# Optimization experiments

Hardware: AMD Instinct MI355X
Metric: run time of the kernel (lower is better)

Reference implementation:

```python
import jax, jax.numpy as jnp
import numpy as np

NODE_DIM = 128; EDGE_DIM = 64; TIME_DIM = 32; HIDDEN = 256; N_LAYERS = 2
K = 20; N_NODES = 100000; B = 8192
IN_DIM = 2 * NODE_DIM + EDGE_DIM + TIME_DIM  # 352


def time2vec(t, w0, b0, w, b):
    # t: [...] -> [..., TIME_DIM]; linear term + sinusoidal terms (Time2Vec)
    t = t[..., None]
    return jnp.concatenate([w0 * t + b0, jnp.sin(w * t + b)], axis=-1)


def msg_mlp(x, W1, b1, W2, b2):
    # TemporalMessageFunction: Linear -> ReLU -> Linear
    return jax.nn.relu(x @ W1 + b1) @ W2 + b2


def gru_cell(x, h, w_ih, w_hh, b_ih, b_hh):
    # torch.nn.GRUCell math, gate order (r, z, n)
    gx = x @ w_ih.T + b_ih
    gh = h @ w_hh.T + b_hh
    rx, zx, nx = jnp.split(gx, 3, axis=-1)
    rh, zh, nh = jnp.split(gh, 3, axis=-1)
    r = jax.nn.sigmoid(rx + rh)
    z = jax.nn.sigmoid(zx + zh)
    n = jnp.tanh(nx + r * nh)
    return (1.0 - z) * n + z * h


def setup_inputs():
    key = jax.random.key(0)
    ks = jax.random.split(key, 24)
    def rn(i, shape, scale=1.0):
        return jax.random.normal(ks[i], shape, dtype=jnp.float32) * scale
    return {
        "src_nodes": jax.random.randint(ks[0], (B,), 0, N_NODES),
        "dst_nodes": jax.random.randint(ks[1], (B,), 0, N_NODES),
        "edge_attrs": rn(2, (B, EDGE_DIM)),
        "timestamps": jax.random.uniform(ks[3], (B,), dtype=jnp.float32) * 1000.0,
        "memory": rn(4, (N_NODES, NODE_DIM), 0.1),
        "neighbor_ids": jax.random.randint(ks[5], (N_NODES, K), 0, N_NODES),
        "neighbor_times": jax.random.uniform(ks[6], (N_NODES, K), dtype=jnp.float32) * 1000.0,
        "neighbor_edge_attrs": rn(7, (N_NODES, K, EDGE_DIM), 0.1),
        "t2v_w0": rn(8, (1,)),
        "t2v_b0": rn(9, (1,)),
        "t2v_w": rn(10, (TIME_DIM - 1,)),
        "t2v_b": rn(11, (TIME_DIM - 1,)),
        "enc_W": rn(12, (EDGE_DIM, EDGE_DIM), EDGE_DIM ** -0.5),
        "enc_b": rn(13, (EDGE_DIM,), 0.01),
        "mlp_W1": rn(14, (N_LAYERS, IN_DIM, HIDDEN), IN_DIM ** -0.5),
        "mlp_b1": rn(15, (N_LAYERS, HIDDEN), 0.01),
        "mlp_W2": rn(16, (N_LAYERS, HIDDEN, NODE_DIM), HIDDEN ** -0.5),
        "mlp_b2": rn(17, (N_LAYERS, NODE_DIM), 0.01),
        "gru_w_ih": rn(18, (3 * NODE_DIM, NODE_DIM), NODE_DIM ** -0.5),
        "gru_w_hh": rn(19, (3 * NODE_DIM, NODE_DIM), NODE_DIM ** -0.5),
        "gru_b_ih": rn(20, (3 * NODE_DIM,), 0.01),
        "gru_b_hh": rn(21, (3 * NODE_DIM,), 0.01),
    }


def reference(src_nodes, dst_nodes, edge_attrs, timestamps, memory,
              neighbor_ids, neighbor_times, neighbor_edge_attrs,
              t2v_w0, t2v_b0, t2v_w, t2v_b, enc_W, enc_b,
              mlp_W1, mlp_b1, mlp_W2, mlp_b2,
              gru_w_ih, gru_w_hh, gru_b_ih, gru_b_hh):
    time_emb = time2vec(timestamps, t2v_w0, t2v_b0, t2v_w, t2v_b)  # [B, T]
    edge_enc = edge_attrs @ enc_W + enc_b                           # [B, E]
    src_emb = memory[src_nodes]                                     # [B, D]
    dst_emb = memory[dst_nodes]                                     # [B, D]

    def neighbor_agg(node_ids, layer):
        # gather K temporal neighbors per node, run message MLP, mean-aggregate
        nb_ids = neighbor_ids[node_ids]                 # [B, K]
        nb_emb = memory[nb_ids]                         # [B, K, D]
        node_mem = jnp.broadcast_to(memory[node_ids][:, None, :], nb_emb.shape)
        nb_t = time2vec(neighbor_times[node_ids], t2v_w0, t2v_b0, t2v_w, t2v_b)  # [B, K, T]
        nb_e = neighbor_edge_attrs[node_ids]            # [B, K, E]
        x = jnp.concatenate([nb_emb, node_mem, nb_e, nb_t], axis=-1)  # [B, K, IN_DIM]
        msgs = msg_mlp(x, mlp_W1[layer], mlp_b1[layer], mlp_W2[layer], mlp_b2[layer])
        return msgs.mean(axis=1)                        # [B, D]

    for l in range(N_LAYERS):
        src_nb = neighbor_agg(src_nodes, l)
        dst_nb = neighbor_agg(dst_nodes, l)
        x_src = jnp.concatenate([src_emb, dst_emb, edge_enc, time_emb], axis=-1)
        x_dst = jnp.concatenate([dst_emb, src_emb, edge_enc, time_emb], axis=-1)
        m_src = msg_mlp(x_src, mlp_W1[l], mlp_b1[l], mlp_W2[l], mlp_b2[l]) + src_nb
        m_dst = msg_mlp(x_dst, mlp_W1[l], mlp_b1[l], mlp_W2[l], mlp_b2[l]) + dst_nb
        src_emb = gru_cell(m_src, src_emb, gru_w_ih, gru_w_hh, gru_b_ih, gru_b_hh)
        dst_emb = gru_cell(m_dst, dst_emb, gru_w_ih, gru_w_hh, gru_b_ih, gru_b_hh)

    return jnp.concatenate([src_emb, dst_emb], axis=-1)  # [B, 2*D]
```

## Files before the change

### kernel.cpp

```cpp
#include <hip/hip_runtime.h>
#include <math.h>


typedef __bf16 bf16;
typedef __bf16 bf16x8 __attribute__((ext_vector_type(8)));
typedef float f32x4 __attribute__((ext_vector_type(4)));

#define MFMA16(a, b, c) __builtin_amdgcn_mfma_f32_16x16x32_bf16((a), (b), (c), 0, 0, 0)

__device__ __forceinline__ void split2(float v, bf16& hi, bf16& lo) {
  hi = (bf16)v;
  lo = (bf16)(v - (float)hi);
}

__device__ __forceinline__ bf16x8 cvt8(const float* __restrict__ p) {
  float4 a = *(const float4*)p;
  float4 b = *(const float4*)(p + 4);
  bf16x8 r;
  r[0] = (bf16)a.x; r[1] = (bf16)a.y; r[2] = (bf16)a.z; r[3] = (bf16)a.w;
  r[4] = (bf16)b.x; r[5] = (bf16)b.y; r[6] = (bf16)b.z; r[7] = (bf16)b.w;
  return r;
}

#define NB_EV 8192
#define ROWS_NB (NB_EV * 20)
#define N_NODES 100000
#define IN_DIM 352
#define HID 256
#define ND 128

__global__ void k_prep_weights(const float* __restrict__ W1, const float* __restrict__ W2,
                               const float* __restrict__ wih, const float* __restrict__ whh,
                               bf16* __restrict__ W1blk, bf16* __restrict__ W1red,
                               bf16* __restrict__ W2blk,
                               bf16* __restrict__ wihblk, bf16* __restrict__ whhblk,
                               float* __restrict__ w320) {
  const int NW1 = 2 * 11 * 256 * 32;
  const int NW1R = 2 * 7 * 256 * 32;
  const int NW2 = 2 * 2 * 8 * 128 * 32;
  const int NG = 2 * 4 * 384 * 32;
  int total = NW1 + NW1R + NW2 + NG + NG + 512;
  for (int i = blockIdx.x * blockDim.x + threadIdx.x; i < total; i += gridDim.x * blockDim.x) {
    int j = i;
    if (j < NW1) {
      int l = j / 90112, r = j - l * 90112;
      int k0 = r / 8192, r2 = r & 8191;
      int n = r2 >> 5, ko = r2 & 31, k = k0 * 32 + ko;
      W1blk[j] = (bf16)W1[(l * 352 + k) * 256 + n];
    } else if ((j -= NW1) < NW1R) {
      int l = j / 57344, r = j - l * 57344;
      int kq = r / 8192, r2 = r & 8191;
      int n = r2 >> 5, ko = r2 & 31;
      int k = (kq < 4) ? (kq * 32 + ko) : ((kq < 6) ? (256 + (kq - 4) * 32 + ko) : (320 + ko));
      W1red[j] = (bf16)W1[(l * 352 + k) * 256 + n];
    } else if ((j -= NW1R) < NW2) {
      int l = j >> 16, r = j & 65535;
      int plane = r >> 15, r2 = r & 32767;
      int kg = r2 >> 12, r3 = r2 & 4095;
      int n = r3 >> 5, ko = r3 & 31, k = kg * 32 + ko;
      bf16 hi, lo; split2(W2[(l * 256 + k) * 128 + n], hi, lo);
      W2blk[j] = plane ? lo : hi;
    } else if ((j -= NW2) < NG) {
      int plane = j / 49152, r = j - plane * 49152;
      int kg = r / 12288, r2 = r - kg * 12288;
      int n = r2 >> 5, ko = r2 & 31, k = kg * 32 + ko;
      bf16 hi, lo; split2(wih[n * 128 + k], hi, lo);
      wihblk[j] = plane ? lo : hi;
    } else if ((j -= NG) < NG) {
      int plane = j / 49152, r = j - plane * 49152;
      int kg = r / 12288, r2 = r - kg * 12288;
      int n = r2 >> 5, ko = r2 & 31, k = kg * 32 + ko;
      bf16 hi, lo; split2(whh[n * 128 + k], hi, lo);
      whhblk[j] = plane ? lo : hi;
    } else {
      j -= NG;
      int l = j >> 8, n = j & 255;
      w320[j] = W1[(l * 352 + 320) * 256 + n];
    }
  }
}

__global__ void k_prep_misc(const float* __restrict__ ts, const float* __restrict__ w0,
                            const float* __restrict__ b0, const float* __restrict__ w,
                            const float* __restrict__ bb,
                            const int* __restrict__ srcn, const int* __restrict__ dstn,
                            const float* __restrict__ memory,
                            float* __restrict__ time_emb, float* __restrict__ embA0,
                            float* __restrict__ embB0) {
  const int N1 = NB_EV * 32, N2 = NB_EV * ND;
  int total = N1 + N2;
  float w0v = w0[0], b0v = b0[0];
  for (int i = blockIdx.x * blockDim.x + threadIdx.x; i < total; i += gridDim.x * blockDim.x) {
    int j = i;
    if (j < N1) {
      int b = j >> 5, c = j & 31;
      float t = ts[b];
      time_emb[j] = (c == 0) ? (w0v * t + b0v) : sinf(w[c - 1] * t + bb[c - 1]);
    } else {
      j -= N1;
      int b = j >> 7, c = j & 127;
      embA0[j] = memory[(long)srcn[b] * ND + c];
      embB0[j] = memory[(long)dstn[b] * ND + c];
    }
  }
}

__global__ void k_prep_mem(const float* __restrict__ memory, bf16* __restrict__ memB) {
  long total = (long)N_NODES * ND / 8;
  for (long i = blockIdx.x * blockDim.x + threadIdx.x; i < total; i += (long)gridDim.x * blockDim.x) {
    bf16x8 v = cvt8(memory + i * 8);
    *(bf16x8*)&memB[i * 8] = v;
  }
}

__global__ __launch_bounds__(256) void k_prep_nbr(
    const int* __restrict__ srcn, const int* __restrict__ dstn,
    const int* __restrict__ nbids, const float* __restrict__ nbt,
    const float* __restrict__ nbe,
    const float* __restrict__ w0p, const float* __restrict__ b0p,
    const float* __restrict__ wp, const float* __restrict__ bp,
    bf16* __restrict__ Xlin, int* __restrict__ nbidArr, float* __restrict__ clArr) {
  __shared__ int flat_l[64];
  __shared__ float t_l[64];
  const int tid = threadIdx.x;
  const int side = blockIdx.y;
  const int r0 = blockIdx.x * 64;
  const int* nodes = side ? dstn : srcn;
  if (tid < 64) {
    int rg = r0 + tid;
    int b = rg / 20, k = rg - b * 20;
    int n = nodes[b];
    int flat = n * 20 + k;
    flat_l[tid] = flat;
    nbidArr[side * ROWS_NB + rg] = nbids[flat];
    float t = nbt[flat];
    t_l[tid] = t;
    clArr[side * ROWS_NB + rg] = w0p[0] * t + b0p[0];
  }
  __syncthreads();
  for (int task = tid; task < 64 * 12; task += 256) {
    int r = task / 12, j = task - r * 12;
    bf16x8 v;
    if (j < 8) {
      v = cvt8(nbe + (long)flat_l[r] * 64 + j * 8);
    } else {
      float t = t_l[r];
#pragma unroll
      for (int q = 0; q < 8; ++q) {
        int c = (j - 8) * 8 + q;
        v[q] = (c == 0) ? (bf16)0.f : (bf16)__sinf(wp[c - 1] * t + bp[c - 1]);
      }
    }
    *(bf16x8*)&Xlin[((long)side * ROWS_NB + r0 + r) * 96 + j * 8] = v;
  }
}

__global__ void k_edge(const float* __restrict__ ea, const float* __restrict__ encW,
                       const float* __restrict__ encb, float* __restrict__ out) {
  __shared__ float row[64];
  int b = blockIdx.x, j = threadIdx.x;
  row[j] = ea[b * 64 + j];
  __syncthreads();
  float s = encb[j];
#pragma unroll
  for (int k = 0; k < 64; ++k) s += row[k] * encW[k * 64 + j];
  out[b * 64 + j] = s;
}

__global__ __launch_bounds__(256) void k_hnode(
    const int* __restrict__ srcn, const int* __restrict__ dstn,
    const float* __restrict__ memory, const bf16* __restrict__ W1blk,
    float* __restrict__ Hnode) {
  const int tid = threadIdx.x;
  const int wid = tid >> 6, lane = tid & 63;
  const int colq = lane & 15, cq = lane >> 4;
  const int cq8 = cq * 8;
  const int z = blockIdx.y, layer = z >> 1, side = z & 1;
  const int b0 = blockIdx.x * 64;
  const int* nodes = side ? dstn : srcn;

  long node_r[4];
#pragma unroll
  for (int nr = 0; nr < 4; ++nr) node_r[nr] = nodes[b0 + nr * 16 + colq];

  const bf16* W1l = W1blk + layer * 90112 + 4 * 8192 + (wid * 16 + colq) * 32 + cq8;
  f32x4 acc[4][4];
#pragma unroll
  for (int mc = 0; mc < 4; ++mc)
#pragma unroll
    for (int nr = 0; nr < 4; ++nr) acc[mc][nr] = (f32x4){0.f, 0.f, 0.f, 0.f};
#pragma unroll
  for (int k0 = 0; k0 < 4; ++k0) {
    bf16x8 xb[4];
#pragma unroll
    for (int nr = 0; nr < 4; ++nr)
      xb[nr] = cvt8(memory + node_r[nr] * ND + k0 * 32 + cq8);
    bf16x8 wf[4];
#pragma unroll
    for (int mc = 0; mc < 4; ++mc)
      wf[mc] = *(const bf16x8*)(W1l + k0 * 8192 + mc * 2048);
#pragma unroll
    for (int mc = 0; mc < 4; ++mc)
#pragma unroll
      for (int nr = 0; nr < 4; ++nr)
        acc[mc][nr] = MFMA16(wf[mc], xb[nr], acc[mc][nr]);
  }
#pragma unroll
  for (int mc = 0; mc < 4; ++mc)
#pragma unroll
    for (int nr = 0; nr < 4; ++nr) {
      long row = (long)z * NB_EV + b0 + nr * 16 + colq;
      *(f32x4*)&Hnode[row * 256 + mc * 64 + wid * 16 + cq * 4] = acc[mc][nr];
    }
}

#define HSS2 136
#define F_XS 0
#define F_HHI 35840
#define F_HLO 57600
#define F_CL 79360
#define F_TOT 79680
__global__ __launch_bounds__(256, 2) void k_nbr(
    const bf16* __restrict__ memB, const int* __restrict__ nbidArr,
    const float* __restrict__ clArr, const bf16* __restrict__ Xlin,
    const float* __restrict__ Hnode,
    const bf16* __restrict__ W1red, const bf16* __restrict__ W2blk,
    const float* __restrict__ w320, const float* __restrict__ b1,
    const float* __restrict__ b2, float* __restrict__ nb_out) {
  __shared__ __align__(16) char smem[F_TOT];
  bf16* xs = (bf16*)(smem + F_XS);
  bf16* hhi = (bf16*)(smem + F_HHI);
  bf16* hlo = (bf16*)(smem + F_HLO);
  float* cl = (float*)(smem + F_CL);
  int* nbid_l = (int*)(smem + F_HHI);

  const int tid = threadIdx.x;
  const int wid = tid >> 6, lane = tid & 63;
  const int colq = lane & 15, cq = lane >> 4;
  const int cq8 = cq * 8;
  const int side = blockIdx.y;
  const int r0 = blockIdx.x * 80;

  if (tid < 80) {
    nbid_l[tid] = nbidArr[side * ROWS_NB + r0 + tid];
    cl[tid] = clArr[side * ROWS_NB + r0 + tid];
  }
  __syncthreads();

  float clr[5];
  int ev_r[5];
#pragma unroll
  for (int nr = 0; nr < 5; ++nr) {
    int row = nr * 16 + colq;
    clr[nr] = cl[row];
    ev_r[nr] = blockIdx.x * 4 + row / 20;
  }

  for (int task = tid; task < 80 * 28; task += 256) {
    int r = task / 28, c16 = task - r * 28;
    bf16x8 v;
    int kq, k8;
    if (c16 < 16) {
      v = *(const bf16x8*)&memB[(long)nbid_l[r] * ND + c16 * 8];
      kq = c16 >> 2; k8 = c16 & 3;
    } else {
      int jj = c16 - 16;
      v = *(const bf16x8*)&Xlin[((long)side * ROWS_NB + r0 + r) * 96 + jj * 8];
      kq = (jj < 8) ? (4 + (jj >> 2)) : 6;
      k8 = (jj < 8) ? (jj & 3) : (jj - 8);
    }
    int swz = k8 ^ (r & 3) ^ ((r >> 2) & 3);
    *(bf16x8*)&xs[kq * 2560 + r * 32 + swz * 8] = v;
  }
  __syncthreads();

  const int swzr = cq ^ (colq & 3) ^ ((colq >> 2) & 3);

#pragma unroll
  for (int layer = 0; layer < 2; ++layer) {
    const bf16* W1l = W1red + layer * 57344 + (wid * 16 + colq) * 32 + cq8;
    const float* Hz = Hnode + ((long)(layer * 2 + side) * NB_EV) * 256;

    f32x4 acc[4][5];
#pragma unroll
    for (int mc = 0; mc < 4; ++mc)
#pragma unroll
      for (int nr = 0; nr < 5; ++nr)
        acc[mc][nr] = *(const f32x4*)&Hz[(long)ev_r[nr] * 256 + mc * 64 + wid * 16 + cq * 4];

    bf16x8 w1f[7][4];
#pragma unroll
    for (int kq = 0; kq < 7; ++kq)
#pragma unroll
      for (int mc = 0; mc < 4; ++mc)
        w1f[kq][mc] = *(const bf16x8*)(W1l + kq * 8192 + mc * 2048);
#pragma unroll
    for (int kq = 0; kq < 7; ++kq)
#pragma unroll
      for (int mc = 0; mc < 4; ++mc)
        asm volatile("" : "+v"(w1f[kq][mc]));

#pragma unroll
    for (int kq = 0; kq < 7; ++kq) {
      bf16x8 xb[5];
#pragma unroll
      for (int nr = 0; nr < 5; ++nr)
        xb[nr] = *(const bf16x8*)(xs + kq * 2560 + (nr * 16 + colq) * 32 + swzr * 8);
#pragma unroll
      for (int mc = 0; mc < 4; ++mc)
#pragma unroll
        for (int nr = 0; nr < 5; ++nr)
          acc[mc][nr] = MFMA16(w1f[kq][mc], xb[nr], acc[mc][nr]);
    }

    const float* w320l = w320 + layer * 256;
    const float* b1l = b1 + layer * 256;
#pragma unroll
    for (int mc = 0; mc < 4; ++mc) {
      int c0 = mc * 64 + wid * 16 + cq * 4;
      float4 wv = *(const float4*)&w320l[c0];
      float4 bv = *(const float4*)&b1l[c0];
#pragma unroll
      for (int nr = 0; nr < 5; ++nr) {
        float c = clr[nr];
        acc[mc][nr][0] = fmaxf(acc[mc][nr][0] + c * wv.x + bv.x, 0.f);
        acc[mc][nr][1] = fmaxf(acc[mc][nr][1] + c * wv.y + bv.y, 0.f);
        acc[mc][nr][2] = fmaxf(acc[mc][nr][2] + c * wv.z + bv.z, 0.f);
        acc[mc][nr][3] = fmaxf(acc[mc][nr][3] + c * wv.w + bv.w, 0.f);
      }
    }

    if (layer == 1) __syncthreads();

    const bf16* W2h = W2blk + layer * 65536 + (wid * 32 + colq) * 32 + cq8;
    const bf16* W2l = W2h + 32768;
    f32x4 acc2[2][5];
#pragma unroll
    for (int mc2 = 0; mc2 < 2; ++mc2)
#pragma unroll
      for (int nr = 0; nr < 5; ++nr) acc2[mc2][nr] = (f32x4){0.f, 0.f, 0.f, 0.f};

#pragma unroll
    for (int hh = 0; hh < 2; ++hh) {
#pragma unroll
      for (int mq = 0; mq < 2; ++mq) {
        int mc = hh * 2 + mq;
        int cl0 = mq * 64 + wid * 16 + cq * 4;
#pragma unroll
        for (int nr = 0; nr < 5; ++nr) {
          int r = nr * 16 + colq;
          union { bf16 h[4]; uint2 u; } ph, pl;
#pragma unroll
          for (int i = 0; i < 4; ++i) split2(acc[mc][nr][i], ph.h[i], pl.h[i]);
          *(uint2*)&hhi[r * HSS2 + cl0] = ph.u;
          *(uint2*)&hlo[r * HSS2 + cl0] = pl.u;
        }
      }
      __syncthreads();

      bf16x8 w2hf[4][2], w2lf[4][2];
#pragma unroll
      for (int kq = 0; kq < 4; ++kq)
#pragma unroll
        for (int mc2 = 0; mc2 < 2; ++mc2) {
          w2hf[kq][mc2] = *(const bf16x8*)(W2h + (hh * 4 + kq) * 4096 + mc2 * 512);
          w2lf[kq][mc2] = *(const bf16x8*)(W2l + (hh * 4 + kq) * 4096 + mc2 * 512);
        }
#pragma unroll
      for (int kq = 0; kq < 4; ++kq)
#pragma unroll
        for (int mc2 = 0; mc2 < 2; ++mc2) {
          asm volatile("" : "+v"(w2hf[kq][mc2]));
          asm volatile("" : "+v"(w2lf[kq][mc2]));
        }

#pragma unroll
      for (int kq = 0; kq < 4; ++kq) {
        bf16x8 bh[5], bl[5];
#pragma unroll
        for (int nr = 0; nr < 5; ++nr) {
          int r = nr * 16 + colq;
          bh[nr] = *(const bf16x8*)(hhi + r * HSS2 + kq * 32 + cq8);
          bl[nr] = *(const bf16x8*)(hlo + r * HSS2 + kq * 32 + cq8);
        }
#pragma unroll
        for (int mc2 = 0; mc2 < 2; ++mc2)
#pragma unroll
          for (int nr = 0; nr < 5; ++nr) {
            acc2[mc2][nr] = MFMA16(w2hf[kq][mc2], bh[nr], acc2[mc2][nr]);
            acc2[mc2][nr] = MFMA16(w2lf[kq][mc2], bh[nr], acc2[mc2][nr]);
            acc2[mc2][nr] = MFMA16(w2hf[kq][mc2], bl[nr], acc2[mc2][nr]);
          }
      }
      if (hh == 0) __syncthreads();
    }

    {
      const float* b2l = b2 + layer * 128;
      long zbase = (long)(layer * 2 + side) * NB_EV * ND;
#pragma unroll
      for (int e = 0; e < 4; ++e) {
        int lo = e * 20, hi = lo + 20;
        f32x4 v[2];
#pragma unroll
        for (int mc2 = 0; mc2 < 2; ++mc2) {
          v[mc2] = (f32x4){0.f, 0.f, 0.f, 0.f};
#pragma unroll
          for (int nr = 0; nr < 5; ++nr) {
            int rl = nr * 16 + colq;
            if (rl >= lo && rl < hi) v[mc2] += acc2[mc2][nr];
          }
        }
#pragma unroll
        for (int s = 1; s < 16; s <<= 1) {
#pragma unroll
          for (int mc2 = 0; mc2 < 2; ++mc2) {
            v[mc2][0] += __shfl_xor(v[mc2][0], s);
            v[mc2][1] += __shfl_xor(v[mc2][1], s);
            v[mc2][2] += __shfl_xor(v[mc2][2], s);
            v[mc2][3] += __shfl_xor(v[mc2][3], s);
          }
        }
        if (colq == e) {
          long b = blockIdx.x * 4 + e;
#pragma unroll
          for (int mc2 = 0; mc2 < 2; ++mc2) {
            int c = wid * 32 + mc2 * 16 + cq * 4;
            float4 bv = *(const float4*)&b2l[c];
            float4 o;
            o.x = (v[mc2][0] + 20.f * bv.x) * 0.05f;
            o.y = (v[mc2][1] + 20.f * bv.y) * 0.05f;
            o.z = (v[mc2][2] + 20.f * bv.z) * 0.05f;
            o.w = (v[mc2][3] + 20.f * bv.w) * 0.05f;
            *(float4*)&nb_out[zbase + b * ND + c] = o;
          }
        }
      }
    }
  }
}

#define XSS 360
#define HSS 136
#define E_G 46080
#define E_CL 80896
#define E_TOT 81152
__global__ __launch_bounds__(256, 1) void k_event(
    int layer, const float* __restrict__ embA_in, const float* __restrict__ embB_in,
    float* __restrict__ outA, int ostrideA, float* __restrict__ outB, int ostrideB,
    const float* __restrict__ time_emb, const float* __restrict__ edge_enc,
    const bf16* __restrict__ W1blk, const bf16* __restrict__ W2blk,
    const float* __restrict__ w320, const float* __restrict__ b1,
    const float* __restrict__ b2, const float* __restrict__ nb_out,
    const bf16* __restrict__ wihblk, const bf16* __restrict__ whhblk,
    const float* __restrict__ bih, const float* __restrict__ bhh) {
  __shared__ __align__(16) char smem[E_TOT];
  bf16* xs = (bf16*)(smem);
  bf16* hhi = (bf16*)(smem);
  bf16* hlo = (bf16*)(smem + 17408);
  bf16* mhi = (bf16*)(smem);
  bf16* mlo = (bf16*)(smem + 17408);
  bf16* ghi = (bf16*)(smem + E_G);
  bf16* glo = (bf16*)(smem + E_G + 17408);
  float* cl = (float*)(smem + E_CL);

  const int tid = threadIdx.x;
  const int r0 = blockIdx.x * 64;
  const int side = r0 >> 13;
  const int b0r = r0 & (NB_EV - 1);
  const float* ea = side ? embB_in : embA_in;
  const float* eb = side ? embA_in : embB_in;

  if (tid < 64) cl[tid] = time_emb[(b0r + tid) * 32];

  for (int task = tid; task < 64 * 88; task += 256) {
    int r = task / 88; int c = (task - r * 88) * 4;
    int b = b0r + r;
    float4 v;
    if (c < 128) {
      v = *(const float4*)&ea[(long)b * ND + c];
      bf16 h0, l0, h1, l1, h2, l2, h3, l3;
      split2(v.x, h0, l0); split2(v.y, h1, l1); split2(v.z, h2, l2); split2(v.w, h3, l3);
      ghi[r * HSS + c + 0] = h0; glo[r * HSS + c + 0] = l0;
      ghi[r * HSS + c + 1] = h1; glo[r * HSS + c + 1] = l1;
      ghi[r * HSS + c + 2] = h2; glo[r * HSS + c + 2] = l2;
      ghi[r * HSS + c + 3] = h3; glo[r * HSS + c + 3] = l3;
    } else if (c < 256) {
      v = *(const float4*)&eb[(long)b * ND + (c - 128)];
    } else if (c < 320) {
      v = *(const float4*)&edge_enc[(long)b * 64 + (c - 256)];
    } else {
      float vv[4];
#pragma unroll
      for (int q = 0; q < 4; ++q) {
        int cc = c + q - 320;
        vv[q] = (cc == 0) ? 0.f : time_emb[b * 32 + cc];
      }
      v = make_float4(vv[0], vv[1], vv[2], vv[3]);
    }
    union { bf16 h[4]; uint2 u; } pk;
    pk.h[0] = (bf16)v.x; pk.h[1] = (bf16)v.y; pk.h[2] = (bf16)v.z; pk.h[3] = (bf16)v.w;
    *(uint2*)&xs[r * XSS + c] = pk.u;
  }
  __syncthreads();

  const int wid = tid >> 6, lane = tid & 63;
  const int colq = lane & 15, cq = lane >> 4;
  const int rsub = cq * 4;

  const bf16* W1l = W1blk + layer * 90112 + (wid * 64 + colq) * 32 + cq * 8;
  const bf16* xsl = xs + colq * XSS + cq * 8;
  f32x4 acc[4][4];
#pragma unroll
  for (int m = 0; m < 4; ++m)
#pragma unroll
    for (int n = 0; n < 4; ++n) acc[m][n] = (f32x4){0.f, 0.f, 0.f, 0.f};
#pragma unroll
  for (int k0 = 0; k0 < 11; ++k0) {
    bf16x8 a[4], b[4];
#pragma unroll
    for (int m = 0; m < 4; ++m) a[m] = *(const bf16x8*)(xsl + m * 16 * XSS + k0 * 32);
#pragma unroll
    for (int n = 0; n < 4; ++n) b[n] = *(const bf16x8*)(W1l + k0 * 8192 + n * 512);
#pragma unroll
    for (int m = 0; m < 4; ++m)
#pragma unroll
      for (int n = 0; n < 4; ++n) acc[m][n] = MFMA16(a[m], b[n], acc[m][n]);
  }
  __syncthreads();

  const float* w320l = w320 + layer * 256;
  const float* b1l = b1 + layer * 256;
#pragma unroll
  for (int n = 0; n < 4; ++n) {
    int cg = wid * 64 + n * 16 + colq;
    float wv = w320l[cg], bv = b1l[cg];
#pragma unroll
    for (int m = 0; m < 4; ++m)
#pragma unroll
      for (int i = 0; i < 4; ++i) {
        int r = m * 16 + rsub + i;
        acc[m][n][i] = fmaxf(acc[m][n][i] + cl[r] * wv + bv, 0.f);
      }
  }
  if (wid < 2) {
#pragma unroll
    for (int m = 0; m < 4; ++m)
#pragma unroll
      for (int n = 0; n < 4; ++n)
#pragma unroll
        for (int i = 0; i < 4; ++i) {
          int r = m * 16 + rsub + i;
          int cc = wid * 64 + n * 16 + colq;
          bf16 hi, lo; split2(acc[m][n][i], hi, lo);
          hhi[r * HSS + cc] = hi;
          hlo[r * HSS + cc] = lo;
        }
  }
  __syncthreads();

  const bf16* W2h = W2blk + layer * 65536 + (wid * 32 + colq) * 32 + cq * 8;
  const bf16* W2l = W2h + 32768;
  const bf16* hhil = hhi + colq * HSS + cq * 8;
  const bf16* hlol = hlo + colq * HSS + cq * 8;
  f32x4 acc2[4][2];
#pragma unroll
  for (int m = 0; m < 4; ++m)
#pragma unroll
    for (int n = 0; n < 2; ++n) acc2[m][n] = (f32x4){0.f, 0.f, 0.f, 0.f};
#pragma unroll
  for (int kg = 0; kg < 8; ++kg) {
    if (kg == 4) {
      __syncthreads();
      if (wid >= 2) {
#pragma unroll
        for (int m = 0; m < 4; ++m)
#pragma unroll
          for (int n = 0; n < 4; ++n)
#pragma unroll
            for (int i = 0; i < 4; ++i) {
              int r = m * 16 + rsub + i;
              int cc = (wid & 1) * 64 + n * 16 + colq;
              bf16 hi, lo; split2(acc[m][n][i], hi, lo);
              hhi[r * HSS + cc] = hi;
              hlo[r * HSS + cc] = lo;
            }
      }
      __syncthreads();
    }
    int lk = (kg & 3) * 32;
    bf16x8 ahi[4], alo[4], bhi[2], blo[2];
#pragma unroll
    for (int m = 0; m < 4; ++m) {
      ahi[m] = *(const bf16x8*)(hhil + m * 16 * HSS + lk);
      alo[m] = *(const bf16x8*)(hlol + m * 16 * HSS + lk);
    }
#pragma unroll
    for (int n = 0; n < 2; ++n) {
      bhi[n] = *(const bf16x8*)(W2h + kg * 4096 + n * 512);
      blo[n] = *(const bf16x8*)(W2l + kg * 4096 + n * 512);
    }
#pragma unroll
    for (int m = 0; m < 4; ++m)
#pragma unroll
      for (int n = 0; n < 2; ++n) {
        acc2[m][n] = MFMA16(ahi[m], bhi[n], acc2[m][n]);
        acc2[m][n] = MFMA16(ahi[m], blo[n], acc2[m][n]);
        acc2[m][n] = MFMA16(alo[m], bhi[n], acc2[m][n]);
      }
  }
  __syncthreads();

  const float* b2l = b2 + layer * 128;
  const float* nbl = nb_out + ((long)(layer * 2 + side)) * NB_EV * ND;
#pragma unroll
  for (int n = 0; n < 2; ++n) {
    int cg = wid * 32 + n * 16 + colq;
    float bv = b2l[cg];
#pragma unroll
    for (int m = 0; m < 4; ++m)
#pragma unroll
      for (int i = 0; i < 4; ++i) {
        int r = m * 16 + rsub + i;
        float mval = acc2[m][n][i] + bv + nbl[(long)(b0r + r) * ND + cg];
        bf16 hi, lo; split2(mval, hi, lo);
        mhi[r * HSS + cg] = hi;
        mlo[r * HSS + cg] = lo;
      }
  }
  __syncthreads();

  float* outP = side ? outB : outA;
  const int ostride = side ? ostrideB : ostrideA;
  const int rowA = wid * 16 + colq;
  const int rbase = wid * 16 + rsub;
  const bf16* mhil = mhi + rowA * HSS + cq * 8;
  const bf16* mlol = mlo + rowA * HSS + cq * 8;
  const bf16* ghil = ghi + rowA * HSS + cq * 8;
  const bf16* glol = glo + rowA * HSS + cq * 8;
  const bf16* wihl = wihblk + colq * 32 + cq * 8;
  const bf16* whhl = whhblk + colq * 32 + cq * 8;

  for (int jt = 0; jt < 8; ++jt) {
    f32x4 gx[3], gh[3];
#pragma unroll
    for (int g = 0; g < 3; ++g) {
      gx[g] = (f32x4){0.f, 0.f, 0.f, 0.f};
      gh[g] = (f32x4){0.f, 0.f, 0.f, 0.f};
    }
#pragma unroll
    for (int kc = 0; kc < 4; ++kc) {
      bf16x8 amh = *(const bf16x8*)(mhil + kc * 32);
      bf16x8 aml = *(const bf16x8*)(mlol + kc * 32);
      bf16x8 ahh = *(const bf16x8*)(ghil + kc * 32);
      bf16x8 ahl = *(const bf16x8*)(glol + kc * 32);
#pragma unroll
      for (int g = 0; g < 3; ++g) {
        int nb = (g * 128 + jt * 16) * 32;
        bf16x8 bh = *(const bf16x8*)(wihl + kc * 12288 + nb);
        bf16x8 bl = *(const bf16x8*)(wihl + 49152 + kc * 12288 + nb);
        gx[g] = MFMA16(amh, bh, gx[g]);
        gx[g] = MFMA16(aml, bh, gx[g]);
        gx[g] = MFMA16(amh, bl, gx[g]);
        bf16x8 ch = *(const bf16x8*)(whhl + kc * 12288 + nb);
        bf16x8 cl2 = *(const bf16x8*)(whhl + 49152 + kc * 12288 + nb);
        gh[g] = MFMA16(ahh, ch, gh[g]);
        gh[g] = MFMA16(ahl, ch, gh[g]);
        gh[g] = MFMA16(ahh, cl2, gh[g]);
      }
    }
    int j = jt * 16 + colq;
    float bihr = bih[j], bihz = bih[128 + j], bihn = bih[256 + j];
    float bhhr = bhh[j], bhhz = bhh[128 + j], bhhn = bhh[256 + j];
#pragma unroll
    for (int i = 0; i < 4; ++i) {
      int rr = rbase + i;
      float rx = gx[0][i] + bihr, zx = gx[1][i] + bihz, nx = gx[2][i] + bihn;
      float rh = gh[0][i] + bhhr, zh = gh[1][i] + bhhz, nh = gh[2][i] + bhhn;
      float r = 1.f / (1.f + expf(-(rx + rh)));
      float zz = 1.f / (1.f + expf(-(zx + zh)));
      float n = tanhf(nx + r * nh);
      float hval = (float)ghi[rr * HSS + j] + (float)glo[rr * HSS + j];
      outP[(long)(b0r + rr) * ostride + j] = (1.f - zz) * n + zz * hval;
    }
  }
}

extern "C" void kernel_launch(void* const* d_in, const int* in_sizes, int n_in,
                              void* d_out, int out_size, void* d_ws, size_t ws_size,
                              hipStream_t stream) {
  const int* srcn = (const int*)d_in[0];
  const int* dstn = (const int*)d_in[1];
  const float* edge_attrs = (const float*)d_in[2];
  const float* timestamps = (const float*)d_in[3];
  const float* memory = (const float*)d_in[4];
  const int* neighbor_ids = (const int*)d_in[5];
  const float* neighbor_times = (const float*)d_in[6];
  const float* neighbor_edge_attrs = (const float*)d_in[7];
  const float* t2v_w0 = (const float*)d_in[8];
  const float* t2v_b0 = (const float*)d_in[9];
  const float* t2v_w = (const float*)d_in[10];
  const float* t2v_b = (const float*)d_in[11];
  const float* enc_W = (const float*)d_in[12];
  const float* enc_b = (const float*)d_in[13];
  const float* mlp_W1 = (const float*)d_in[14];
  const float* mlp_b1 = (const float*)d_in[15];
  const float* mlp_W2 = (const float*)d_in[16];
  const float* mlp_b2 = (const float*)d_in[17];
  const float* gru_w_ih = (const float*)d_in[18];
  const float* gru_w_hh = (const float*)d_in[19];
  const float* gru_b_ih = (const float*)d_in[20];
  const float* gru_b_hh = (const float*)d_in[21];

  char* ws = (char*)d_ws;
  size_t off = 0;
  auto alloc = [&](size_t bytes) { size_t o = off; off += (bytes + 255) & ~(size_t)255; return o; };
  bf16* W1blk = (bf16*)(ws + alloc((size_t)2 * 11 * 256 * 32 * 2));
  bf16* W1red = (bf16*)(ws + alloc((size_t)2 * 7 * 256 * 32 * 2));
  bf16* W2blk = (bf16*)(ws + alloc((size_t)2 * 2 * 8 * 128 * 32 * 2));
  bf16* wihblk = (bf16*)(ws + alloc((size_t)2 * 4 * 384 * 32 * 2));
  bf16* whhblk = (bf16*)(ws + alloc((size_t)2 * 4 * 384 * 32 * 2));
  float* w320 = (float*)(ws + alloc(512 * 4));
  float* time_emb = (float*)(ws + alloc((size_t)NB_EV * 32 * 4));
  float* edge_enc = (float*)(ws + alloc((size_t)NB_EV * 64 * 4));
  float* embA0 = (float*)(ws + alloc((size_t)NB_EV * ND * 4));
  float* embB0 = (float*)(ws + alloc((size_t)NB_EV * ND * 4));
  float* embA1 = (float*)(ws + alloc((size_t)NB_EV * ND * 4));
  float* embB1 = (float*)(ws + alloc((size_t)NB_EV * ND * 4));
  float* nb_out = (float*)(ws + alloc((size_t)4 * NB_EV * ND * 4));
  float* Hnode = (float*)(ws + alloc((size_t)4 * NB_EV * 256 * 4));
  bf16* memB = (bf16*)(ws + alloc((size_t)N_NODES * ND * 2));
  bf16* Xlin = (bf16*)(ws + alloc((size_t)2 * ROWS_NB * 96 * 2));
  int* nbidArr = (int*)(ws + alloc((size_t)2 * ROWS_NB * 4));
  float* clArr = (float*)(ws + alloc((size_t)2 * ROWS_NB * 4));

  k_prep_weights<<<512, 256, 0, stream>>>(mlp_W1, mlp_W2, gru_w_ih, gru_w_hh,
                                          W1blk, W1red, W2blk, wihblk, whhblk, w320);
  k_prep_misc<<<1024, 256, 0, stream>>>(timestamps, t2v_w0, t2v_b0, t2v_w, t2v_b,
                                        srcn, dstn, memory, time_emb, embA0, embB0);
  k_prep_mem<<<2048, 256, 0, stream>>>(memory, memB);
  k_prep_nbr<<<dim3(2560, 2, 1), 256, 0, stream>>>(
      srcn, dstn, neighbor_ids, neighbor_times, neighbor_edge_attrs,
      t2v_w0, t2v_b0, t2v_w, t2v_b, Xlin, nbidArr, clArr);
  k_edge<<<NB_EV, 64, 0, stream>>>(edge_attrs, enc_W, enc_b, edge_enc);
  k_hnode<<<dim3(128, 4, 1), 256, 0, stream>>>(srcn, dstn, memory, W1blk, Hnode);

  k_nbr<<<dim3(ROWS_NB / 80, 2, 1), 256, 0, stream>>>(
      memB, nbidArr, clArr, Xlin, Hnode, W1red, W2blk, w320, mlp_b1, mlp_b2, nb_out);

  k_event<<<2 * NB_EV / 64, 256, 0, stream>>>(
      0, embA0, embB0, embA1, ND, embB1, ND, time_emb, edge_enc,
      W1blk, W2blk, w320, mlp_b1, mlp_b2, nb_out,
      wihblk, whhblk, gru_b_ih, gru_b_hh);

  float* outf = (float*)d_out;
  k_event<<<2 * NB_EV / 64, 256, 0, stream>>>(
      1, embA1, embB1, outf, 2 * ND, outf + ND, 2 * ND, time_emb, edge_enc,
      W1blk, W2blk, w320, mlp_b1, mlp_b2, nb_out,
      wihblk, whhblk, gru_b_ih, gru_b_hh);
}
```

Measured before the change: 529.7 us.

## Merge prep kernels into one launch and stage neighbor tiles via global_load_lds

Folds the weight-prep, misc-prep, memory bf16 conversion and edge-encoder kernels into a single grid-stride kernel, cutting three launches and their gaps. Separately, the neighbor kernel's LDS fill now uses direct global-to-LDS 16-byte loads with the swizzle moved to the source address, skipping the trip through registers. The fused edge encoder loses its shared-memory row staging and reads encW per element from global memory, and the direct LDS loads rely on lane-contiguous destination addressing being correct.

```diff
diff --git a/kernel.cpp b/kernel.cpp
--- a/kernel.cpp
+++ b/kernel.cpp
@@ -22,6 +22,12 @@
   return r;
 }
 
+typedef const __attribute__((address_space(1))) unsigned int* gptr_t;
+typedef __attribute__((address_space(3))) unsigned int* lptr_t;
+__device__ __forceinline__ void stage16(const void* g, void* l) {
+  __builtin_amdgcn_global_load_lds((gptr_t)g, (lptr_t)l, 16, 0, 0);
+}
+
 #define NB_EV 8192
 #define ROWS_NB (NB_EV * 20)
 #define N_NODES 100000
@@ -29,17 +35,32 @@
 #define HID 256
 #define ND 128
 
-__global__ void k_prep_weights(const float* __restrict__ W1, const float* __restrict__ W2,
-                               const float* __restrict__ wih, const float* __restrict__ whh,
-                               bf16* __restrict__ W1blk, bf16* __restrict__ W1red,
-                               bf16* __restrict__ W2blk,
-                               bf16* __restrict__ wihblk, bf16* __restrict__ whhblk,
-                               float* __restrict__ w320) {
+__global__ void k_prep_all(const float* __restrict__ W1, const float* __restrict__ W2,
+                           const float* __restrict__ wih, const float* __restrict__ whh,
+                           const float* __restrict__ ts, const float* __restrict__ w0,
+                           const float* __restrict__ b0, const float* __restrict__ w,
+                           const float* __restrict__ bb,
+                           const int* __restrict__ srcn, const int* __restrict__ dstn,
+                           const float* __restrict__ memory,
+                           const float* __restrict__ ea, const float* __restrict__ encW,
+                           const float* __restrict__ encb,
+                           bf16* __restrict__ W1blk, bf16* __restrict__ W1red,
+                           bf16* __restrict__ W2blk,
+                           bf16* __restrict__ wihblk, bf16* __restrict__ whhblk,
+                           float* __restrict__ w320,
+                           float* __restrict__ time_emb, float* __restrict__ embA0,
+                           float* __restrict__ embB0, bf16* __restrict__ memB,
+                           float* __restrict__ edge_enc) {
   const int NW1 = 2 * 11 * 256 * 32;
   const int NW1R = 2 * 7 * 256 * 32;
   const int NW2 = 2 * 2 * 8 * 128 * 32;
   const int NG = 2 * 4 * 384 * 32;
-  int total = NW1 + NW1R + NW2 + NG + NG + 512;
+  const int NT = NB_EV * 32;
+  const int NE = NB_EV * ND;
+  const int NM = N_NODES * ND / 8;
+  const int NEE = NB_EV * 64;
+  int total = NW1 + NW1R + NW2 + NG + NG + 512 + NT + NE + NM + NEE;
+  float w0v = w0[0], b0v = b0[0];
   for (int i = blockIdx.x * blockDim.x + threadIdx.x; i < total; i += gridDim.x * blockDim.x) {
     int j = i;
     if (j < NW1) {
@@ -72,44 +93,29 @@
       int n = r2 >> 5, ko = r2 & 31, k = kg * 32 + ko;
       bf16 hi, lo; split2(whh[n * 128 + k], hi, lo);
       whhblk[j] = plane ? lo : hi;
-    } else {
-      j -= NG;
+    } else if ((j -= NG) < 512) {
       int l = j >> 8, n = j & 255;
       w320[j] = W1[(l * 352 + 320) * 256 + n];
-    }
-  }
-}
-
-__global__ void k_prep_misc(const float* __restrict__ ts, const float* __restrict__ w0,
-                            const float* __restrict__ b0, const float* __restrict__ w,
-                            const float* __restrict__ bb,
-                            const int* __restrict__ srcn, const int* __restrict__ dstn,
-                            const float* __restrict__ memory,
-                            float* __restrict__ time_emb, float* __restrict__ embA0,
-                            float* __restrict__ embB0) {
-  const int N1 = NB_EV * 32, N2 = NB_EV * ND;
-  int total = N1 + N2;
-  float w0v = w0[0], b0v = b0[0];
-  for (int i = blockIdx.x * blockDim.x + threadIdx.x; i < total; i += gridDim.x * blockDim.x) {
-    int j = i;
-    if (j < N1) {
+    } else if ((j -= 512) < NT) {
       int b = j >> 5, c = j & 31;
       float t = ts[b];
       time_emb[j] = (c == 0) ? (w0v * t + b0v) : sinf(w[c - 1] * t + bb[c - 1]);
-    } else {
-      j -= N1;
+    } else if ((j -= NT) < NE) {
       int b = j >> 7, c = j & 127;
       embA0[j] = memory[(long)srcn[b] * ND + c];
       embB0[j] = memory[(long)dstn[b] * ND + c];
-    }
-  }
-}
-
-__global__ void k_prep_mem(const float* __restrict__ memory, bf16* __restrict__ memB) {
-  long total = (long)N_NODES * ND / 8;
-  for (long i = blockIdx.x * blockDim.x + threadIdx.x; i < total; i += (long)gridDim.x * blockDim.x) {
-    bf16x8 v = cvt8(memory + i * 8);
-    *(bf16x8*)&memB[i * 8] = v;
+    } else if ((j -= NE) < NM) {
+      bf16x8 v = cvt8(memory + (long)j * 8);
+      *(bf16x8*)&memB[(long)j * 8] = v;
+    } else {
+      j -= NM;
+      int b = j >> 6, c = j & 63;
+      float s = encb[c];
+      const float* row = ea + b * 64;
+#pragma unroll 8
+      for (int k = 0; k < 64; ++k) s += row[k] * encW[k * 64 + c];
+      edge_enc[j] = s;
+    }
   }
 }
 
@@ -155,18 +161,6 @@
   }
 }
 
-__global__ void k_edge(const float* __restrict__ ea, const float* __restrict__ encW,
-                       const float* __restrict__ encb, float* __restrict__ out) {
-  __shared__ float row[64];
-  int b = blockIdx.x, j = threadIdx.x;
-  row[j] = ea[b * 64 + j];
-  __syncthreads();
-  float s = encb[j];
-#pragma unroll
-  for (int k = 0; k < 64; ++k) s += row[k] * encW[k * 64 + j];
-  out[b * 64 + j] = s;
-}
-
 __global__ __launch_bounds__(256) void k_hnode(
     const int* __restrict__ srcn, const int* __restrict__ dstn,
     const float* __restrict__ memory, const bf16* __restrict__ W1blk,
@@ -256,21 +250,25 @@
     ev_r[nr] = blockIdx.x * 4 + row / 20;
   }
 
-  for (int task = tid; task < 80 * 28; task += 256) {
-    int r = task / 28, c16 = task - r * 28;
-    bf16x8 v;
-    int kq, k8;
-    if (c16 < 16) {
-      v = *(const bf16x8*)&memB[(long)nbid_l[r] * ND + c16 * 8];
-      kq = c16 >> 2; k8 = c16 & 3;
-    } else {
-      int jj = c16 - 16;
-      v = *(const bf16x8*)&Xlin[((long)side * ROWS_NB + r0 + r) * 96 + jj * 8];
-      kq = (jj < 8) ? (4 + (jj >> 2)) : 6;
-      k8 = (jj < 8) ? (jj & 3) : (jj - 8);
-    }
-    int swz = k8 ^ (r & 3) ^ ((r >> 2) & 3);
-    *(bf16x8*)&xs[kq * 2560 + r * 32 + swz * 8] = v;
+  {
+    const long xrow = (long)side * ROWS_NB + r0;
+#pragma unroll
+    for (int q = 0; q < 9; ++q) {
+      int i = wid + q * 4;
+      if (i >= 35) break;
+      int s = i * 64 + lane;
+      int kq = s / 320, rem = s - kq * 320;
+      int r = rem >> 2, swz = rem & 3;
+      int k8 = swz ^ (r & 3) ^ ((r >> 2) & 3);
+      const bf16* src;
+      if (kq < 4) {
+        src = memB + (long)nbid_l[r] * ND + (kq * 4 + k8) * 8;
+      } else {
+        int jj = (kq < 6) ? ((kq - 4) * 4 + k8) : (8 + k8);
+        src = Xlin + (xrow + r) * 96 + jj * 8;
+      }
+      stage16(src, (char*)xs + s * 16);
+    }
   }
   __syncthreads();
 
@@ -734,15 +732,15 @@
   int* nbidArr = (int*)(ws + alloc((size_t)2 * ROWS_NB * 4));
   float* clArr = (float*)(ws + alloc((size_t)2 * ROWS_NB * 4));
 
-  k_prep_weights<<<512, 256, 0, stream>>>(mlp_W1, mlp_W2, gru_w_ih, gru_w_hh,
-                                          W1blk, W1red, W2blk, wihblk, whhblk, w320);
-  k_prep_misc<<<1024, 256, 0, stream>>>(timestamps, t2v_w0, t2v_b0, t2v_w, t2v_b,
-                                        srcn, dstn, memory, time_emb, embA0, embB0);
-  k_prep_mem<<<2048, 256, 0, stream>>>(memory, memB);
+  k_prep_all<<<2048, 256, 0, stream>>>(
+      mlp_W1, mlp_W2, gru_w_ih, gru_w_hh,
+      timestamps, t2v_w0, t2v_b0, t2v_w, t2v_b,
+      srcn, dstn, memory, edge_attrs, enc_W, enc_b,
+      W1blk, W1red, W2blk, wihblk, whhblk, w320,
+      time_emb, embA0, embB0, memB, edge_enc);
   k_prep_nbr<<<dim3(2560, 2, 1), 256, 0, stream>>>(
       srcn, dstn, neighbor_ids, neighbor_times, neighbor_edge_attrs,
       t2v_w0, t2v_b0, t2v_w, t2v_b, Xlin, nbidArr, clArr);
-  k_edge<<<NB_EV, 64, 0, stream>>>(edge_attrs, enc_W, enc_b, edge_enc);
   k_hnode<<<dim3(128, 4, 1), 256, 0, stream>>>(srcn, dstn, memory, W1blk, Hnode);
 
   k_nbr<<<dim3(ROWS_NB / 80, 2, 1), 256, 0, stream>>>(
```

Measured after the change: 498.4 us (median of 2 runs). -5.9%, faster.
